# Kernel tuning notes

Measured on AMD Instinct MI355X. Metric: run time of the kernel, lower is better.

## Reference

```python
import jax, jax.numpy as jnp
import numpy as np

N_NODES = 50000
NEG_SLOPE = 0.2  # PyG GATConv default leaky_relu slope


def gat_conv(x, src, dst, W, a_src, a_dst, b):
    """One PyG-style GATConv (concat heads, add_self_loops already applied).
    x: [N, F_in]; W: [H*C, F_in]; a_src/a_dst: [H, C]; b: [H*C]."""
    N = x.shape[0]
    H, C = a_src.shape
    h = (x @ W.T).reshape(N, H, C)                       # [N,H,C]
    alpha_src = jnp.einsum('nhc,hc->nh', h, a_src)       # [N,H]
    alpha_dst = jnp.einsum('nhc,hc->nh', h, a_dst)       # [N,H]
    e = alpha_src[src] + alpha_dst[dst]                  # [E,H]
    e = jax.nn.leaky_relu(e, NEG_SLOPE)
    # segment softmax over incoming edges of each dst node, per head
    m = jax.ops.segment_max(e, dst, num_segments=N)      # [N,H]
    w = jnp.exp(e - m[dst])                              # [E,H]
    s = jax.ops.segment_sum(w, dst, num_segments=N)      # [N,H]
    alpha = w / (s[dst] + 1e-16)                         # [E,H]
    msg = alpha[:, :, None] * h[src]                     # [E,H,C]
    out = jax.ops.segment_sum(msg, dst, num_segments=N)  # [N,H,C]
    return out.reshape(N, H * C) + b


def setup_inputs() -> dict:
    key = jax.random.key(0)
    ks = jax.random.split(key, 8)
    N, E, F_in, H, C, L = N_NODES, 800000, 128, 4, 32, 3
    x = jax.random.normal(ks[0], (N, F_in), dtype=jnp.float32)
    edge_index = jax.random.randint(ks[1], (2, E), 0, N, dtype=jnp.int32)
    Ws = jax.random.normal(ks[2], (L, H * C, F_in), dtype=jnp.float32) * 0.1
    att_src = jax.random.normal(ks[3], (L, H, C), dtype=jnp.float32) * 0.1
    att_dst = jax.random.normal(ks[4], (L, H, C), dtype=jnp.float32) * 0.1
    conv_bias = jnp.zeros((L, H * C), dtype=jnp.float32)
    Wf = jax.random.normal(ks[5], (32, H * C), dtype=jnp.float32) * 0.1
    bf = jnp.zeros((32,), dtype=jnp.float32)
    return {"x": x, "Ws": Ws, "att_src": att_src, "att_dst": att_dst,
            "conv_bias": conv_bias, "Wf": Wf, "bf": bf, "edge_index": edge_index}


def reference(x, Ws, att_src, att_dst, conv_bias, Wf, bf, edge_index):
    N = x.shape[0]
    # PyG GATConv add_self_loops=True (default): append i->i for every node
    loop = jnp.arange(N, dtype=edge_index.dtype)
    src = jnp.concatenate([edge_index[0], loop])
    dst = jnp.concatenate([edge_index[1], loop])
    for l in range(Ws.shape[0]):
        x = gat_conv(x, src, dst, Ws[l], att_src[l], att_dst[l], conv_bias[l])
        x = jax.nn.relu(x)
        # F.dropout(p=0.1, training=False) is identity in eval mode
    return x @ Wf.T + bf
```

## Files before the change

kernel.cpp:

```cpp
#include <hip/hip_runtime.h>
#include <hip/hip_bf16.h>
#include <math.h>

#define N_NODES 50000
#define NE      800000
#define F       128
#define NHEAD   4
#define NEG     0.2f

#define CAP 64
#define GM 32
#define GGEMM ((N_NODES + GM - 1) / GM)

#define NPART  256
#define ECHUNK ((NE + NPART - 1) / NPART)
#define NBKT   ((N_NODES + 255) / 256)
#define SUBCAP 64

typedef __attribute__((ext_vector_type(8))) short bf16x8;
typedef __attribute__((ext_vector_type(4))) float f32x4;
typedef _Float16 f16x8 __attribute__((ext_vector_type(8)));


__device__ __forceinline__ unsigned short f2bf(float x) {
    unsigned int u = __float_as_uint(x);
    u += 0x7FFFu + ((u >> 16) & 1u);
    return (unsigned short)(u >> 16);
}
__device__ __forceinline__ float bf2f(unsigned short h) {
    return __uint_as_float(((unsigned int)h) << 16);
}
__device__ __forceinline__ void cvt8(float4 a, float4 b, bf16x8* hi, bf16x8* lo) {
    float f[8] = {a.x, a.y, a.z, a.w, b.x, b.y, b.z, b.w};
    bf16x8 h, l;
#pragma unroll
    for (int j = 0; j < 8; j++) {
        unsigned short hu = f2bf(f[j]);
        h[j] = (short)hu;
        l[j] = (short)f2bf(f[j] - bf2f(hu));
    }
    *hi = h; *lo = l;
}
__device__ __forceinline__ void cvt8h(float4 a, float4 b, f16x8* hi, f16x8* lo) {
    float f[8] = {a.x, a.y, a.z, a.w, b.x, b.y, b.z, b.w};
    f16x8 h, l;
#pragma unroll
    for (int j = 0; j < 8; j++) {
        _Float16 hh = (_Float16)f[j];
        h[j] = hh;
        l[j] = (_Float16)(f[j] - (float)hh);
    }
    *hi = h; *lo = l;
}

__device__ __forceinline__ int lds_unit(int m, int q) {
    return 4 * m + (q ^ ((m >> 1) & 3));
}


__global__ __launch_bounds__(256) void k_gemm_part(
        const float* __restrict__ X,
        const float* __restrict__ W,
        const float* __restrict__ a_s,
        const float* __restrict__ a_d,
        _Float16* __restrict__ hout,
        float* __restrict__ asrc,
        float* __restrict__ adst,
        const int* __restrict__ ei,
        unsigned int* __restrict__ bkt,
        int* __restrict__ cnt2) {
    __shared__ short Ah[128 * 8], Al[128 * 8];
    __shared__ short Bh[512 * 8], Bl[512 * 8];
    __shared__ int pcnt[NBKT];
    int tid = threadIdx.x;

    if (blockIdx.x < NPART) {
        int blk = blockIdx.x;
        if (tid < NBKT) pcnt[tid] = 0;
        __syncthreads();
        int start = blk * ECHUNK;
        int end = start + ECHUNK; if (end > NE) end = NE;
        for (int i = start + tid; i < end; i += 256) {
            unsigned s = (unsigned)ei[i];
            unsigned d = (unsigned)ei[NE + i];
            int b = (int)(d >> 8);
            int r = atomicAdd(&pcnt[b], 1);
            if (r < SUBCAP)
                bkt[(size_t)(b * NPART + blk) * SUBCAP + r] = (d << 16) | s;
        }
        __syncthreads();
        if (tid < NBKT) cnt2[tid * NPART + blk] = pcnt[tid];
        return;
    }

    int bm = (blockIdx.x - NPART) * GM;

    bool aT = (tid < 128);
    int am = tid >> 2, aq = tid & 3;
    int xunit = ((am >> 4) << 6) + lds_unit(am & 15, aq);
    int wj = tid >> 2, wq = tid & 3;
    int wunit = ((wj >> 4) << 6) + lds_unit(wj & 15, wq);

    int lane = tid & 63, wv = tid >> 6;
    int rg = wv & 1, cg = wv >> 1;
    int fm = lane & 15, fq = lane >> 4;
    int a_unit = (rg << 6) + lds_unit(fm, fq);
    int b_unit0 = lds_unit(fm, fq);

    f32x4 acc[4];
#pragma unroll
    for (int nt = 0; nt < 4; nt++) acc[nt] = (f32x4){0.f, 0.f, 0.f, 0.f};

    float4 xp0, xp1, wp0, wp1, wp2, wp3;
    int gr = bm + am;
    bool xok = aT && (gr < N_NODES);
    const float* xrow = X + (size_t)gr * F + aq * 8;
    const float* wrow1 = W + (size_t)wj * F + wq * 8;
    const float* wrow2 = W + (size_t)(wj + 64) * F + wq * 8;
    float4 z4 = make_float4(0.f, 0.f, 0.f, 0.f);

    auto load_tile = [&](int k0) {
        xp0 = xok ? *(const float4*)(xrow + k0)     : z4;
        xp1 = xok ? *(const float4*)(xrow + k0 + 4) : z4;
        wp0 = *(const float4*)(wrow1 + k0);
        wp1 = *(const float4*)(wrow1 + k0 + 4);
        wp2 = *(const float4*)(wrow2 + k0);
        wp3 = *(const float4*)(wrow2 + k0 + 4);
    };
    auto store_tile = [&]() {
        bf16x8 hi, lo;
        if (aT) {
            cvt8(xp0, xp1, &hi, &lo);
            *(bf16x8*)&Ah[xunit * 8] = hi;  *(bf16x8*)&Al[xunit * 8] = lo;
        }
        cvt8(wp0, wp1, &hi, &lo);
        *(bf16x8*)&Bh[wunit * 8] = hi;  *(bf16x8*)&Bl[wunit * 8] = lo;
        cvt8(wp2, wp3, &hi, &lo);
        *(bf16x8*)&Bh[(wunit + 256) * 8] = hi;  *(bf16x8*)&Bl[(wunit + 256) * 8] = lo;
    };

    load_tile(0);
    store_tile();
    __syncthreads();

#pragma unroll
    for (int t = 0; t < 4; t++) {
        if (t < 3) load_tile((t + 1) * 32);
        bf16x8 ah = *(bf16x8*)&Ah[a_unit * 8];
        bf16x8 al = *(bf16x8*)&Al[a_unit * 8];
#pragma unroll
        for (int nt = 0; nt < 4; nt++) {
            int bu = ((((cg << 2) + nt) << 6) + b_unit0) * 8;
            bf16x8 bh = *(bf16x8*)&Bh[bu];
            bf16x8 bl = *(bf16x8*)&Bl[bu];
            acc[nt] = __builtin_amdgcn_mfma_f32_16x16x32_bf16(ah, bh, acc[nt], 0, 0, 0);
            acc[nt] = __builtin_amdgcn_mfma_f32_16x16x32_bf16(ah, bl, acc[nt], 0, 0, 0);
            acc[nt] = __builtin_amdgcn_mfma_f32_16x16x32_bf16(al, bh, acc[nt], 0, 0, 0);
        }
        __syncthreads();
        if (t < 3) { store_tile(); __syncthreads(); }
    }

    float as_v[4], ad_v[4];
#pragma unroll
    for (int nt = 0; nt < 4; nt++) {
        as_v[nt] = a_s[((cg << 2) + nt) * 16 + fm];
        ad_v[nt] = a_d[((cg << 2) + nt) * 16 + fm];
    }
#pragma unroll
    for (int r = 0; r < 4; r++) {
        int n = bm + rg * 16 + fq * 4 + r;
        bool ok = (n < N_NODES);
        if (ok) {
#pragma unroll
            for (int nt = 0; nt < 4; nt++)
                hout[(size_t)n * F + ((cg << 2) + nt) * 16 + fm] = (_Float16)acc[nt][r];
        }
        float ps[2], pd[2];
#pragma unroll
        for (int hh = 0; hh < 2; hh++) {
            ps[hh] = acc[2 * hh][r] * as_v[2 * hh] + acc[2 * hh + 1][r] * as_v[2 * hh + 1];
            pd[hh] = acc[2 * hh][r] * ad_v[2 * hh] + acc[2 * hh + 1][r] * ad_v[2 * hh + 1];
        }
#pragma unroll
        for (int s = 1; s < 16; s <<= 1) {
#pragma unroll
            for (int hh = 0; hh < 2; hh++) {
                ps[hh] += __shfl_xor(ps[hh], s);
                pd[hh] += __shfl_xor(pd[hh], s);
            }
        }
        if (ok && fm == 0) {
            *(float2*)&asrc[n * 4 + cg * 2] = make_float2(ps[0], ps[1]);
            *(float2*)&adst[n * 4 + cg * 2] = make_float2(pd[0], pd[1]);
        }
    }
}


__global__ __launch_bounds__(256) void k_place(const unsigned int* __restrict__ bkt,
                                               const int* __restrict__ cnt2,
                                               int* __restrict__ deg,
                                               int* __restrict__ col) {
    __shared__ int cnt[256];
    int b = blockIdx.x;
    int t = threadIdx.x;
    cnt[t] = 0;
    __syncthreads();
    int c = cnt2[b * NPART + t];
    if (c > SUBCAP) c = SUBCAP;
    const unsigned int* seg = bkt + (size_t)(b * NPART + t) * SUBCAP;
    for (int j = 0; j < c; j++) {
        unsigned int e = seg[j];
        int d = (int)(e >> 16), s = (int)(e & 0xFFFFu);
        int r = atomicAdd(&cnt[d & 255], 1);
        if (r < CAP - 1) col[d * CAP + r] = s;
    }
    __syncthreads();
    int node = (b << 8) + t;
    if (node < N_NODES) {
        int r = cnt[t];
        if (r > CAP - 1) r = CAP - 1;
        col[node * CAP + r] = node;
        deg[node] = r + 1;
    }
}


__global__ __launch_bounds__(256) void k_gemm16(const _Float16* __restrict__ X,
                                                const float* __restrict__ W,
                                                const float* __restrict__ a_s,
                                                const float* __restrict__ a_d,
                                                _Float16* __restrict__ hout,
                                                float* __restrict__ asrc,
                                                float* __restrict__ adst) {
    __shared__ _Float16 Ahf[128 * 8];
    __shared__ _Float16 Bhf[512 * 8], Blf[512 * 8];
    int tid = threadIdx.x;
    int bm = blockIdx.x * GM;

    bool aT = (tid < 128);
    int am = tid >> 2, aq = tid & 3;
    int xunit = ((am >> 4) << 6) + lds_unit(am & 15, aq);
    int wj = tid >> 2, wq = tid & 3;
    int wunit = ((wj >> 4) << 6) + lds_unit(wj & 15, wq);

    int lane = tid & 63, wv = tid >> 6;
    int rg = wv & 1, cg = wv >> 1;
    int fm = lane & 15, fq = lane >> 4;
    int a_unit = (rg << 6) + lds_unit(fm, fq);
    int b_unit0 = lds_unit(fm, fq);

    f32x4 acc[4];
#pragma unroll
    for (int nt = 0; nt < 4; nt++) acc[nt] = (f32x4){0.f, 0.f, 0.f, 0.f};

    f16x8 xp;
    float4 wp0, wp1, wp2, wp3;
    int gr = bm + am;
    bool xok = aT && (gr < N_NODES);
    const _Float16* xrow = X + (size_t)gr * F + aq * 8;
    const float* wrow1 = W + (size_t)wj * F + wq * 8;
    const float* wrow2 = W + (size_t)(wj + 64) * F + wq * 8;

    auto load_tile = [&](int k0) {
        f16x8 zz = {0, 0, 0, 0, 0, 0, 0, 0};
        xp = xok ? *(const f16x8*)(xrow + k0) : zz;
        wp0 = *(const float4*)(wrow1 + k0);
        wp1 = *(const float4*)(wrow1 + k0 + 4);
        wp2 = *(const float4*)(wrow2 + k0);
        wp3 = *(const float4*)(wrow2 + k0 + 4);
    };
    auto store_tile = [&]() {
        if (aT) *(f16x8*)&Ahf[xunit * 8] = xp;
        f16x8 hi, lo;
        cvt8h(wp0, wp1, &hi, &lo);
        *(f16x8*)&Bhf[wunit * 8] = hi;  *(f16x8*)&Blf[wunit * 8] = lo;
        cvt8h(wp2, wp3, &hi, &lo);
        *(f16x8*)&Bhf[(wunit + 256) * 8] = hi;  *(f16x8*)&Blf[(wunit + 256) * 8] = lo;
    };

    load_tile(0);
    store_tile();
    __syncthreads();

#pragma unroll
    for (int t = 0; t < 4; t++) {
        if (t < 3) load_tile((t + 1) * 32);
        f16x8 ah = *(f16x8*)&Ahf[a_unit * 8];
#pragma unroll
        for (int nt = 0; nt < 4; nt++) {
            int bu = ((((cg << 2) + nt) << 6) + b_unit0) * 8;
            f16x8 bh = *(f16x8*)&Bhf[bu];
            f16x8 bl = *(f16x8*)&Blf[bu];
            acc[nt] = __builtin_amdgcn_mfma_f32_16x16x32_f16(ah, bh, acc[nt], 0, 0, 0);
            acc[nt] = __builtin_amdgcn_mfma_f32_16x16x32_f16(ah, bl, acc[nt], 0, 0, 0);
        }
        __syncthreads();
        if (t < 3) { store_tile(); __syncthreads(); }
    }

    float as_v[4], ad_v[4];
#pragma unroll
    for (int nt = 0; nt < 4; nt++) {
        as_v[nt] = a_s[((cg << 2) + nt) * 16 + fm];
        ad_v[nt] = a_d[((cg << 2) + nt) * 16 + fm];
    }
#pragma unroll
    for (int r = 0; r < 4; r++) {
        int n = bm + rg * 16 + fq * 4 + r;
        bool ok = (n < N_NODES);
        if (ok) {
#pragma unroll
            for (int nt = 0; nt < 4; nt++)
                hout[(size_t)n * F + ((cg << 2) + nt) * 16 + fm] = (_Float16)acc[nt][r];
        }
        float ps[2], pd[2];
#pragma unroll
        for (int hh = 0; hh < 2; hh++) {
            ps[hh] = acc[2 * hh][r] * as_v[2 * hh] + acc[2 * hh + 1][r] * as_v[2 * hh + 1];
            pd[hh] = acc[2 * hh][r] * ad_v[2 * hh] + acc[2 * hh + 1][r] * ad_v[2 * hh + 1];
        }
#pragma unroll
        for (int s = 1; s < 16; s <<= 1) {
#pragma unroll
            for (int hh = 0; hh < 2; hh++) {
                ps[hh] += __shfl_xor(ps[hh], s);
                pd[hh] += __shfl_xor(pd[hh], s);
            }
        }
        if (ok && fm == 0) {
            *(float2*)&asrc[n * 4 + cg * 2] = make_float2(ps[0], ps[1]);
            *(float2*)&adst[n * 4 + cg * 2] = make_float2(pd[0], pd[1]);
        }
    }
}


#define EPAD 68

__global__ __launch_bounds__(256) void k_aggr(const _Float16* __restrict__ h,
                                              const float* __restrict__ asrc,
                                              const float* __restrict__ adst,
                                              const int* __restrict__ deg,
                                              const int* __restrict__ col,
                                              const float* __restrict__ bias,
                                              _Float16* __restrict__ xout) {
    __shared__ int   scol[4][64];
    __shared__ float swT[4][4 * EPAD];
    int wave = threadIdx.x >> 6;
    int lane = threadIdx.x & 63;
    int n = blockIdx.x * 4 + wave;
    if (n >= N_NODES) return;
    int wl = lane & 15;
    int he = lane >> 4;
    int hc = wl >> 2;
    int cnt = deg[n]; if (cnt > CAP) cnt = CAP;
    int beg = n * CAP;
    float4 ad4 = *(const float4*)&adst[n * 4];

    float s_run = 0.f;
    float acc[8];
#pragma unroll
    for (int j = 0; j < 8; j++) acc[j] = 0.f;

    {
        int sidx = 0;
        float4 w4 = make_float4(0.f, 0.f, 0.f, 0.f);
        if (lane < cnt) {
            sidx = col[beg + lane];
            float4 av = *(const float4*)&asrc[sidx * 4];
            float ex = av.x + ad4.x, ey = av.y + ad4.y,
                  ez = av.z + ad4.z, ew = av.w + ad4.w;
            ex = (ex > 0.f) ? ex : NEG * ex;
            ey = (ey > 0.f) ? ey : NEG * ey;
            ez = (ez > 0.f) ? ez : NEG * ez;
            ew = (ew > 0.f) ? ew : NEG * ew;
            w4.x = __expf(ex); w4.y = __expf(ey);
            w4.z = __expf(ez); w4.w = __expf(ew);
        }
        scol[wave][lane] = sidx;
        swT[wave][0 * EPAD + lane] = w4.x;
        swT[wave][1 * EPAD + lane] = w4.y;
        swT[wave][2 * EPAD + lane] = w4.z;
        swT[wave][3 * EPAD + lane] = w4.w;
        __builtin_amdgcn_sched_barrier(0);
        float4 wv4 = *(float4*)&swT[wave][he * EPAD + wl * 4];
        float S = (wv4.x + wv4.y) + (wv4.z + wv4.w);
#pragma unroll
        for (int s = 1; s < 16; s <<= 1) S += __shfl_xor(S, s);
        s_run += S;
        __builtin_amdgcn_sched_barrier(0);
#pragma unroll 2
        for (int p = 0; p < cnt; p += 4) {
            int ep = p + he;
            int s = scol[wave][ep];
            float wgt = swT[wave][hc * EPAD + ep];
            f16x8 hv = *(const f16x8*)&h[(size_t)s * F + wl * 8];
#pragma unroll
            for (int j = 0; j < 8; j++)
                acc[j] = fmaf(wgt, (float)hv[j], acc[j]);
        }
    }

#pragma unroll
    for (int j = 0; j < 8; j++) {
        acc[j] += __shfl_xor(acc[j], 16);
        acc[j] += __shfl_xor(acc[j], 32);
    }
    float sv = __shfl(s_run, hc * 16);
    float inv = 1.f / (sv + 1e-16f);
    float4 b0 = *(const float4*)&bias[wl * 8];
    float4 b1 = *(const float4*)&bias[wl * 8 + 4];
    float bb[8] = {b0.x, b0.y, b0.z, b0.w, b1.x, b1.y, b1.z, b1.w};
    if (he == 0) {
        f16x8 st;
#pragma unroll
        for (int j = 0; j < 8; j++)
            st[j] = (_Float16)fmaxf(fmaf(acc[j], inv, bb[j]), 0.f);
        *(f16x8*)&xout[(size_t)n * F + wl * 8] = st;
    }
}


#define FCB 128

__global__ __launch_bounds__(256) void k_fc(const _Float16* __restrict__ X,
                                            const float* __restrict__ Wf,
                                            const float* __restrict__ bf,
                                            float* __restrict__ out) {
    __shared__ float WsT[128 * 36];
    __shared__ float XsT[32 * 132];
    int tid = threadIdx.x;
    int bm = blockIdx.x * FCB;

#pragma unroll
    for (int u = 0; u < 16; u++) {
        int idx = tid + 256 * u;
        int o = idx & 31, k = idx >> 5;
        WsT[k * 36 + o] = Wf[o * 128 + k];
    }

    int tx = tid & 7;
    int ty = tid >> 3;
    float acc[4][4];
#pragma unroll
    for (int i = 0; i < 4; i++)
#pragma unroll
        for (int j = 0; j < 4; j++) acc[i][j] = 0.f;

    for (int k0 = 0; k0 < 128; k0 += 32) {
        __syncthreads();
#pragma unroll
        for (int u = 0; u < 2; u++) {
            int idx = tid + 256 * u;
            int nn = idx & 127, c = idx >> 7;
            int gn = bm + nn;
            f16x8 v = {0, 0, 0, 0, 0, 0, 0, 0};
            if (gn < N_NODES) v = *(const f16x8*)&X[(size_t)gn * F + k0 + c * 8];
#pragma unroll
            for (int j = 0; j < 8; j++)
                XsT[(c * 8 + j) * 132 + nn] = (float)v[j];
        }
        __syncthreads();

#pragma unroll
        for (int kk = 0; kk < 32; kk++) {
            float4 xv = *(float4*)&XsT[kk * 132 + ty * 4];
            float4 wv = *(float4*)&WsT[(k0 + kk) * 36 + tx * 4];
            float xs[4] = {xv.x, xv.y, xv.z, xv.w};
            float ws[4] = {wv.x, wv.y, wv.z, wv.w};
#pragma unroll
            for (int i = 0; i < 4; i++)
#pragma unroll
                for (int j = 0; j < 4; j++)
                    acc[i][j] = fmaf(xs[i], ws[j], acc[i][j]);
        }
    }

    float4 bv = *(const float4*)&bf[tx * 4];
#pragma unroll
    for (int i = 0; i < 4; i++) {
        int n = bm + ty * 4 + i;
        if (n < N_NODES) {
            float4 o4 = make_float4(acc[i][0] + bv.x, acc[i][1] + bv.y,
                                    acc[i][2] + bv.z, acc[i][3] + bv.w);
            *(float4*)&out[n * 32 + tx * 4] = o4;
        }
    }
}


extern "C" void kernel_launch(void* const* d_in, const int* in_sizes, int n_in,
                              void* d_out, int out_size, void* d_ws, size_t ws_size,
                              hipStream_t stream) {
    const float* x      = (const float*)d_in[0];
    const float* Ws     = (const float*)d_in[1];
    const float* a_src  = (const float*)d_in[2];
    const float* a_dst  = (const float*)d_in[3];
    const float* cbias  = (const float*)d_in[4];
    const float* Wf     = (const float*)d_in[5];
    const float* bf     = (const float*)d_in[6];
    const int*   ei     = (const int*)d_in[7];
    float* out = (float*)d_out;

    char* p = (char*)d_ws;
    auto carve = [&](size_t bytes) {
        char* r = p;
        p += (bytes + 255) & ~(size_t)255;
        return r;
    };
    _Float16* xA   = (_Float16*)carve((size_t)N_NODES * F * 2);
    _Float16* xB   = (_Float16*)carve((size_t)N_NODES * F * 2);
    _Float16* xC   = (_Float16*)carve((size_t)N_NODES * F * 2);
    _Float16* hbuf = (_Float16*)carve((size_t)N_NODES * F * 2);
    float* asrc = (float*)carve((size_t)N_NODES * NHEAD * 4);
    float* adst = (float*)carve((size_t)N_NODES * NHEAD * 4);
    int* deg    = (int*)carve((size_t)N_NODES * 4);
    int* col    = (int*)carve((size_t)N_NODES * CAP * 4);
    unsigned int* bkt = (unsigned int*)carve((size_t)NBKT * NPART * SUBCAP * 4);
    int* cnt2   = (int*)carve((size_t)NBKT * NPART * 4);

    int gaggr = (N_NODES + 3) / 4;

    k_gemm_part<<<NPART + GGEMM, 256, 0, stream>>>(
        x, Ws, a_src, a_dst, hbuf, asrc, adst, ei, bkt, cnt2);
    k_place<<<NBKT, 256, 0, stream>>>(bkt, cnt2, deg, col);
    k_aggr<<<gaggr, 256, 0, stream>>>(hbuf, asrc, adst, deg, col, cbias, xA);

    k_gemm16<<<GGEMM, 256, 0, stream>>>(xA, Ws + (size_t)F * F, a_src + F, a_dst + F,
                                        hbuf, asrc, adst);
    k_aggr<<<gaggr, 256, 0, stream>>>(hbuf, asrc, adst, deg, col, cbias + F, xB);

    k_gemm16<<<GGEMM, 256, 0, stream>>>(xB, Ws + (size_t)2 * F * F, a_src + 2 * F,
                                        a_dst + 2 * F, hbuf, asrc, adst);
    k_aggr<<<gaggr, 256, 0, stream>>>(hbuf, asrc, adst, deg, col, cbias + 2 * F, xC);

    k_fc<<<(N_NODES + FCB - 1) / FCB, 256, 0, stream>>>(xC, Wf, bf, out);
}
```

Baseline: 273.0 us.

## Pre-split weights once and load GEMM fragments directly from global memory

Adds a small prep kernel that converts each layer's fp32 weights once into hi/lo bf16 or fp16 halves. The GEMM kernels then drop their LDS staging, per-block weight conversion and barriers, and read MFMA fragments straight from global or L2. The aggregation loop unroll also goes from 2 to 4. This trades one extra launch and uncoalesced direct fragment loads for less redundant conversion work per block and fewer synchronisations.

```diff
diff --git a/kernel.cpp b/kernel.cpp
--- a/kernel.cpp
+++ b/kernel.cpp
@@ -41,26 +41,37 @@
     }
     *hi = h; *lo = l;
 }
-__device__ __forceinline__ void cvt8h(float4 a, float4 b, f16x8* hi, f16x8* lo) {
-    float f[8] = {a.x, a.y, a.z, a.w, b.x, b.y, b.z, b.w};
-    f16x8 h, l;
-#pragma unroll
-    for (int j = 0; j < 8; j++) {
-        _Float16 hh = (_Float16)f[j];
-        h[j] = hh;
-        l[j] = (_Float16)(f[j] - (float)hh);
-    }
-    *hi = h; *lo = l;
-}
-
-__device__ __forceinline__ int lds_unit(int m, int q) {
-    return 4 * m + (q ^ ((m >> 1) & 3));
+
+
+__global__ __launch_bounds__(256) void k_prep(const float* __restrict__ Ws,
+                                              short* __restrict__ W1h,
+                                              short* __restrict__ W1l,
+                                              _Float16* __restrict__ W2h,
+                                              _Float16* __restrict__ W2l,
+                                              _Float16* __restrict__ W3h,
+                                              _Float16* __restrict__ W3l) {
+    int i = blockIdx.x * 256 + threadIdx.x;
+    if (i >= 3 * F * F) return;
+    float v = Ws[i];
+    int j = i & (F * F - 1);
+    if (i < F * F) {
+        unsigned short h = f2bf(v);
+        W1h[j] = (short)h;
+        W1l[j] = (short)f2bf(v - bf2f(h));
+    } else if (i < 2 * F * F) {
+        _Float16 h = (_Float16)v;
+        W2h[j] = h; W2l[j] = (_Float16)(v - (float)h);
+    } else {
+        _Float16 h = (_Float16)v;
+        W3h[j] = h; W3l[j] = (_Float16)(v - (float)h);
+    }
 }
 
 
 __global__ __launch_bounds__(256) void k_gemm_part(
         const float* __restrict__ X,
-        const float* __restrict__ W,
+        const short* __restrict__ W1h,
+        const short* __restrict__ W1l,
         const float* __restrict__ a_s,
         const float* __restrict__ a_d,
         _Float16* __restrict__ hout,
@@ -69,8 +80,6 @@
         const int* __restrict__ ei,
         unsigned int* __restrict__ bkt,
         int* __restrict__ cnt2) {
-    __shared__ short Ah[128 * 8], Al[128 * 8];
-    __shared__ short Bh[512 * 8], Bl[512 * 8];
     __shared__ int pcnt[NBKT];
     int tid = threadIdx.x;
 
@@ -94,71 +103,35 @@
     }
 
     int bm = (blockIdx.x - NPART) * GM;
-
-    bool aT = (tid < 128);
-    int am = tid >> 2, aq = tid & 3;
-    int xunit = ((am >> 4) << 6) + lds_unit(am & 15, aq);
-    int wj = tid >> 2, wq = tid & 3;
-    int wunit = ((wj >> 4) << 6) + lds_unit(wj & 15, wq);
-
     int lane = tid & 63, wv = tid >> 6;
     int rg = wv & 1, cg = wv >> 1;
     int fm = lane & 15, fq = lane >> 4;
-    int a_unit = (rg << 6) + lds_unit(fm, fq);
-    int b_unit0 = lds_unit(fm, fq);
+
+    int arow = bm + rg * 16 + fm;
+    bool xok = (arow < N_NODES);
+    const float* xrow = X + (size_t)arow * F + fq * 8;
+    float4 z4 = make_float4(0.f, 0.f, 0.f, 0.f);
 
     f32x4 acc[4];
 #pragma unroll
     for (int nt = 0; nt < 4; nt++) acc[nt] = (f32x4){0.f, 0.f, 0.f, 0.f};
 
-    float4 xp0, xp1, wp0, wp1, wp2, wp3;
-    int gr = bm + am;
-    bool xok = aT && (gr < N_NODES);
-    const float* xrow = X + (size_t)gr * F + aq * 8;
-    const float* wrow1 = W + (size_t)wj * F + wq * 8;
-    const float* wrow2 = W + (size_t)(wj + 64) * F + wq * 8;
-    float4 z4 = make_float4(0.f, 0.f, 0.f, 0.f);
-
-    auto load_tile = [&](int k0) {
-        xp0 = xok ? *(const float4*)(xrow + k0)     : z4;
-        xp1 = xok ? *(const float4*)(xrow + k0 + 4) : z4;
-        wp0 = *(const float4*)(wrow1 + k0);
-        wp1 = *(const float4*)(wrow1 + k0 + 4);
-        wp2 = *(const float4*)(wrow2 + k0);
-        wp3 = *(const float4*)(wrow2 + k0 + 4);
-    };
-    auto store_tile = [&]() {
-        bf16x8 hi, lo;
-        if (aT) {
-            cvt8(xp0, xp1, &hi, &lo);
-            *(bf16x8*)&Ah[xunit * 8] = hi;  *(bf16x8*)&Al[xunit * 8] = lo;
-        }
-        cvt8(wp0, wp1, &hi, &lo);
-        *(bf16x8*)&Bh[wunit * 8] = hi;  *(bf16x8*)&Bl[wunit * 8] = lo;
-        cvt8(wp2, wp3, &hi, &lo);
-        *(bf16x8*)&Bh[(wunit + 256) * 8] = hi;  *(bf16x8*)&Bl[(wunit + 256) * 8] = lo;
-    };
-
-    load_tile(0);
-    store_tile();
-    __syncthreads();
-
 #pragma unroll
     for (int t = 0; t < 4; t++) {
-        if (t < 3) load_tile((t + 1) * 32);
-        bf16x8 ah = *(bf16x8*)&Ah[a_unit * 8];
-        bf16x8 al = *(bf16x8*)&Al[a_unit * 8];
+        float4 xa = xok ? *(const float4*)(xrow + t * 32)     : z4;
+        float4 xb = xok ? *(const float4*)(xrow + t * 32 + 4) : z4;
+        bf16x8 ah, al;
+        cvt8(xa, xb, &ah, &al);
 #pragma unroll
         for (int nt = 0; nt < 4; nt++) {
-            int bu = ((((cg << 2) + nt) << 6) + b_unit0) * 8;
-            bf16x8 bh = *(bf16x8*)&Bh[bu];
-            bf16x8 bl = *(bf16x8*)&Bl[bu];
+            int col = ((cg << 2) + nt) * 16 + fm;
+            size_t off = (size_t)col * F + t * 32 + fq * 8;
+            bf16x8 bh = *(const bf16x8*)(W1h + off);
+            bf16x8 bl = *(const bf16x8*)(W1l + off);
             acc[nt] = __builtin_amdgcn_mfma_f32_16x16x32_bf16(ah, bh, acc[nt], 0, 0, 0);
             acc[nt] = __builtin_amdgcn_mfma_f32_16x16x32_bf16(ah, bl, acc[nt], 0, 0, 0);
             acc[nt] = __builtin_amdgcn_mfma_f32_16x16x32_bf16(al, bh, acc[nt], 0, 0, 0);
         }
-        __syncthreads();
-        if (t < 3) { store_tile(); __syncthreads(); }
     }
 
     float as_v[4], ad_v[4];
@@ -228,76 +201,40 @@
 
 
 __global__ __launch_bounds__(256) void k_gemm16(const _Float16* __restrict__ X,
-                                                const float* __restrict__ W,
+                                                const _Float16* __restrict__ Wh,
+                                                const _Float16* __restrict__ Wl,
                                                 const float* __restrict__ a_s,
                                                 const float* __restrict__ a_d,
                                                 _Float16* __restrict__ hout,
                                                 float* __restrict__ asrc,
                                                 float* __restrict__ adst) {
-    __shared__ _Float16 Ahf[128 * 8];
-    __shared__ _Float16 Bhf[512 * 8], Blf[512 * 8];
     int tid = threadIdx.x;
     int bm = blockIdx.x * GM;
-
-    bool aT = (tid < 128);
-    int am = tid >> 2, aq = tid & 3;
-    int xunit = ((am >> 4) << 6) + lds_unit(am & 15, aq);
-    int wj = tid >> 2, wq = tid & 3;
-    int wunit = ((wj >> 4) << 6) + lds_unit(wj & 15, wq);
-
     int lane = tid & 63, wv = tid >> 6;
     int rg = wv & 1, cg = wv >> 1;
     int fm = lane & 15, fq = lane >> 4;
-    int a_unit = (rg << 6) + lds_unit(fm, fq);
-    int b_unit0 = lds_unit(fm, fq);
+
+    int arow = bm + rg * 16 + fm;
+    bool xok = (arow < N_NODES);
+    const _Float16* xrow = X + (size_t)arow * F + fq * 8;
+    f16x8 zz = {0, 0, 0, 0, 0, 0, 0, 0};
 
     f32x4 acc[4];
 #pragma unroll
     for (int nt = 0; nt < 4; nt++) acc[nt] = (f32x4){0.f, 0.f, 0.f, 0.f};
 
-    f16x8 xp;
-    float4 wp0, wp1, wp2, wp3;
-    int gr = bm + am;
-    bool xok = aT && (gr < N_NODES);
-    const _Float16* xrow = X + (size_t)gr * F + aq * 8;
-    const float* wrow1 = W + (size_t)wj * F + wq * 8;
-    const float* wrow2 = W + (size_t)(wj + 64) * F + wq * 8;
-
-    auto load_tile = [&](int k0) {
-        f16x8 zz = {0, 0, 0, 0, 0, 0, 0, 0};
-        xp = xok ? *(const f16x8*)(xrow + k0) : zz;
-        wp0 = *(const float4*)(wrow1 + k0);
-        wp1 = *(const float4*)(wrow1 + k0 + 4);
-        wp2 = *(const float4*)(wrow2 + k0);
-        wp3 = *(const float4*)(wrow2 + k0 + 4);
-    };
-    auto store_tile = [&]() {
-        if (aT) *(f16x8*)&Ahf[xunit * 8] = xp;
-        f16x8 hi, lo;
-        cvt8h(wp0, wp1, &hi, &lo);
-        *(f16x8*)&Bhf[wunit * 8] = hi;  *(f16x8*)&Blf[wunit * 8] = lo;
-        cvt8h(wp2, wp3, &hi, &lo);
-        *(f16x8*)&Bhf[(wunit + 256) * 8] = hi;  *(f16x8*)&Blf[(wunit + 256) * 8] = lo;
-    };
-
-    load_tile(0);
-    store_tile();
-    __syncthreads();
-
 #pragma unroll
     for (int t = 0; t < 4; t++) {
-        if (t < 3) load_tile((t + 1) * 32);
-        f16x8 ah = *(f16x8*)&Ahf[a_unit * 8];
+        f16x8 ah = xok ? *(const f16x8*)(xrow + t * 32) : zz;
 #pragma unroll
         for (int nt = 0; nt < 4; nt++) {
-            int bu = ((((cg << 2) + nt) << 6) + b_unit0) * 8;
-            f16x8 bh = *(f16x8*)&Bhf[bu];
-            f16x8 bl = *(f16x8*)&Blf[bu];
+            int col = ((cg << 2) + nt) * 16 + fm;
+            size_t off = (size_t)col * F + t * 32 + fq * 8;
+            f16x8 bh = *(const f16x8*)(Wh + off);
+            f16x8 bl = *(const f16x8*)(Wl + off);
             acc[nt] = __builtin_amdgcn_mfma_f32_16x16x32_f16(ah, bh, acc[nt], 0, 0, 0);
             acc[nt] = __builtin_amdgcn_mfma_f32_16x16x32_f16(ah, bl, acc[nt], 0, 0, 0);
         }
-        __syncthreads();
-        if (t < 3) { store_tile(); __syncthreads(); }
     }
 
     float as_v[4], ad_v[4];
@@ -391,7 +328,7 @@
         for (int s = 1; s < 16; s <<= 1) S += __shfl_xor(S, s);
         s_run += S;
         __builtin_amdgcn_sched_barrier(0);
-#pragma unroll 2
+#pragma unroll 4
         for (int p = 0; p < cnt; p += 4) {
             int ep = p + he;
             int s = scol[wave][ep];
@@ -520,20 +457,28 @@
     int* col    = (int*)carve((size_t)N_NODES * CAP * 4);
     unsigned int* bkt = (unsigned int*)carve((size_t)NBKT * NPART * SUBCAP * 4);
     int* cnt2   = (int*)carve((size_t)NBKT * NPART * 4);
+    short* W1h  = (short*)carve((size_t)F * F * 2);
+    short* W1l  = (short*)carve((size_t)F * F * 2);
+    _Float16* W2h = (_Float16*)carve((size_t)F * F * 2);
+    _Float16* W2l = (_Float16*)carve((size_t)F * F * 2);
+    _Float16* W3h = (_Float16*)carve((size_t)F * F * 2);
+    _Float16* W3l = (_Float16*)carve((size_t)F * F * 2);
 
     int gaggr = (N_NODES + 3) / 4;
 
+    k_prep<<<(3 * F * F + 255) / 256, 256, 0, stream>>>(Ws, W1h, W1l,
+                                                        W2h, W2l, W3h, W3l);
     k_gemm_part<<<NPART + GGEMM, 256, 0, stream>>>(
-        x, Ws, a_src, a_dst, hbuf, asrc, adst, ei, bkt, cnt2);
+        x, W1h, W1l, a_src, a_dst, hbuf, asrc, adst, ei, bkt, cnt2);
     k_place<<<NBKT, 256, 0, stream>>>(bkt, cnt2, deg, col);
     k_aggr<<<gaggr, 256, 0, stream>>>(hbuf, asrc, adst, deg, col, cbias, xA);
 
-    k_gemm16<<<GGEMM, 256, 0, stream>>>(xA, Ws + (size_t)F * F, a_src + F, a_dst + F,
+    k_gemm16<<<GGEMM, 256, 0, stream>>>(xA, W2h, W2l, a_src + F, a_dst + F,
                                         hbuf, asrc, adst);
     k_aggr<<<gaggr, 256, 0, stream>>>(hbuf, asrc, adst, deg, col, cbias + F, xB);
 
-    k_gemm16<<<GGEMM, 256, 0, stream>>>(xB, Ws + (size_t)2 * F * F, a_src + 2 * F,
-                                        a_dst + 2 * F, hbuf, asrc, adst);
+    k_gemm16<<<GGEMM, 256, 0, stream>>>(xB, W3h, W3l, a_src + 2 * F, a_dst + 2 * F,
+                                        hbuf, asrc, adst);
     k_aggr<<<gaggr, 256, 0, stream>>>(hbuf, asrc, adst, deg, col, cbias + 2 * F, xC);
 
     k_fc<<<(N_NODES + FCB - 1) / FCB, 256, 0, stream>>>(xC, Wf, bf, out);
```

After: 345.8 us. 26.7% more time.
